# Kernel optimization log

Measured on AMD Instinct MI355X. Metric: run time of the kernel, lower is better.

The kernel has to match this reference:

```python
import jax, jax.numpy as jnp
import numpy as np

B, T, E, H = 2, 2048, 1024, 16
DV = E // H
EPS = 1e-5

def _layernorm(x, g, b):
    m = jnp.mean(x, axis=-1, keepdims=True)
    v = jnp.mean((x - m) ** 2, axis=-1, keepdims=True)
    return (x - m) * jax.lax.rsqrt(v + EPS) * g + b

def setup_inputs() -> dict:
    key = jax.random.key(0)
    ks = jax.random.split(key, 10)
    s = lambda fan_in: 1.0 / np.sqrt(fan_in)
    return {
        "x": jax.random.normal(ks[0], (B, T, E), jnp.float32),
        "wq": jax.random.normal(ks[1], (H, E, DV), jnp.float32) * s(E),
        "wk": jax.random.normal(ks[2], (H, E, DV), jnp.float32) * s(E),
        "wv": jax.random.normal(ks[3], (H, E, DV), jnp.float32) * s(E),
        "w_proj": jax.random.normal(ks[4], (E, E), jnp.float32) * s(E),
        "b_proj": jnp.zeros((E,), jnp.float32),
        "w1": jax.random.normal(ks[5], (E, 4 * E), jnp.float32) * s(E),
        "b1": jnp.zeros((4 * E,), jnp.float32),
        "w2": jax.random.normal(ks[6], (4 * E, E), jnp.float32) * s(4 * E),
        "b2": jnp.zeros((E,), jnp.float32),
        "g1": jnp.ones((E,), jnp.float32),
        "be1": jnp.zeros((E,), jnp.float32),
        "g2": jnp.ones((E,), jnp.float32),
        "be2": jnp.zeros((E,), jnp.float32),
    }

def reference(x, wq, wk, wv, w_proj, b_proj, w1, b1, w2, b2, g1, be1, g2, be2):
    Bc, Tc, C = x.shape
    # --- masked multi-head self-attention on pre-LN input ---
    h = _layernorm(x, g1, be1)
    q = jnp.einsum('bte,hed->bhtd', h, wq)
    k = jnp.einsum('bte,hed->bhtd', h, wk)
    v = jnp.einsum('bte,hed->bhtd', h, wv)
    # NOTE: original scales by C**-0.5 where C = full embed dim (not head dim)
    scores = jnp.einsum('bhtd,bhsd->bhts', q, k) * (C ** -0.5)
    causal = jnp.tril(jnp.ones((Tc, Tc), bool))
    scores = jnp.where(causal, scores, jnp.float32(-jnp.inf))
    probs = jax.nn.softmax(scores, axis=-1)  # dropout is identity in eval
    attn = jnp.einsum('bhts,bhsd->bhtd', probs, v)
    attn = attn.transpose(0, 2, 1, 3).reshape(Bc, Tc, C)
    x = x + (attn @ w_proj + b_proj)
    # --- feed-forward ---
    h2 = _layernorm(x, g2, be2)
    ff = jax.nn.relu(h2 @ w1 + b1) @ w2 + b2
    return x + ff
```

## Files before the change

kernel.cpp:

```cpp
#include <hip/hip_runtime.h>
#include <hip/hip_bf16.h>

typedef __bf16 bf16x8 __attribute__((ext_vector_type(8)));
typedef __bf16 bf16x4 __attribute__((ext_vector_type(4)));
typedef float f32x4 __attribute__((ext_vector_type(4)));

#define T_SEQ 2048
#define EMB 1024
#define NH 16
#define DV 64

__device__ __forceinline__ void gload16(const __bf16* g, __bf16* l) {
    __builtin_amdgcn_global_load_lds(
        (const __attribute__((address_space(1))) unsigned int*)g,
        (__attribute__((address_space(3))) unsigned int*)l, 16, 0, 0);
}

__global__ void transpose_cvt(const float* __restrict__ src, __bf16* __restrict__ dst,
                              int R, int C, long src_bstride, long dst_bstride, float scale) {
    __shared__ float tile[32][33];
    const int b = blockIdx.z;
    const float* s = src + (long)b * src_bstride;
    __bf16* d = dst + (long)b * dst_bstride;
    const int c0 = blockIdx.x * 32, r0 = blockIdx.y * 32;
    #pragma unroll
    for (int i = threadIdx.y; i < 32; i += 8)
        tile[i][threadIdx.x] = s[(long)(r0 + i) * C + c0 + threadIdx.x];
    __syncthreads();
    #pragma unroll
    for (int i = threadIdx.y; i < 32; i += 8)
        d[(long)(c0 + i) * R + r0 + threadIdx.x] = (__bf16)(tile[threadIdx.x][i] * scale);
}

__global__ void vt_transpose(const __bf16* __restrict__ qkv, __bf16* __restrict__ Vt) {
    __shared__ __bf16 tile[64][72];
    const int bh = blockIdx.y, b = bh >> 4, h = bh & 15;
    const int t0 = blockIdx.x * 64;
    const __bf16* src = qkv + (long)b * T_SEQ * 3072 + 2048 + h * 64;
    const int tt = threadIdx.x >> 3, seg = threadIdx.x & 7;
    #pragma unroll
    for (int half = 0; half < 2; half++) {
        const int t = half * 32 + tt;
        bf16x8 v = *reinterpret_cast<const bf16x8*>(src + (long)(t0 + t) * 3072 + seg * 8);
        *reinterpret_cast<bf16x8*>(&tile[t][seg * 8]) = v;
    }
    __syncthreads();
    __bf16* dst = Vt + (long)bh * 64 * T_SEQ + t0;
    #pragma unroll
    for (int half = 0; half < 2; half++) {
        const int d = half * 32 + tt;
        bf16x8 v;
        #pragma unroll
        for (int i = 0; i < 8; i++) v[i] = tile[seg * 8 + i][d];
        *reinterpret_cast<bf16x8*>(dst + (long)d * T_SEQ + seg * 8) = v;
    }
}

__global__ void ln_kernel(const float* __restrict__ x, const float* __restrict__ g,
                          const float* __restrict__ be, __bf16* __restrict__ out) {
    const int row = blockIdx.x;
    const float4 xv = reinterpret_cast<const float4*>(x + (long)row * EMB)[threadIdx.x];
    float s = xv.x + xv.y + xv.z + xv.w;
    float sq = xv.x * xv.x + xv.y * xv.y + xv.z * xv.z + xv.w * xv.w;
    #pragma unroll
    for (int off = 32; off; off >>= 1) { s += __shfl_down(s, off); sq += __shfl_down(sq, off); }
    __shared__ float red[8];
    const int w = threadIdx.x >> 6, lane = threadIdx.x & 63;
    if (lane == 0) { red[w] = s; red[4 + w] = sq; }
    __syncthreads();
    if (threadIdx.x == 0) {
        float st = red[0] + red[1] + red[2] + red[3];
        float sqt = red[4] + red[5] + red[6] + red[7];
        float mean = st * (1.0f / EMB);
        float var = sqt * (1.0f / EMB) - mean * mean;
        red[0] = mean; red[1] = rsqrtf(var + 1e-5f);
    }
    __syncthreads();
    const float mean = red[0], rstd = red[1];
    const float4 gv = reinterpret_cast<const float4*>(g)[threadIdx.x];
    const float4 bv = reinterpret_cast<const float4*>(be)[threadIdx.x];
    bf16x4 o;
    o[0] = (__bf16)((xv.x - mean) * rstd * gv.x + bv.x);
    o[1] = (__bf16)((xv.y - mean) * rstd * gv.y + bv.y);
    o[2] = (__bf16)((xv.z - mean) * rstd * gv.z + bv.z);
    o[3] = (__bf16)((xv.w - mean) * rstd * gv.w + bv.w);
    *reinterpret_cast<bf16x4*>(out + (long)row * EMB + threadIdx.x * 4) = o;
}

template <int RELU, int HAS_BIAS>
__global__ __launch_bounds__(512)
void gemm256(const __bf16* __restrict__ A, const __bf16* __restrict__ BT,
             const float* __restrict__ bias, __bf16* __restrict__ outp,
             int M, int N, int K, int nbx) {
    __shared__ __align__(16) __bf16 lds[3][2][256 * 32];
    const int bid = (int)blockIdx.x;
    const int cpx = (int)gridDim.x >> 3;
    const int wg = (bid & 7) * cpx + (bid >> 3);
    const int bx = wg % nbx, by = wg / nbx;
    const int m0 = by * 256, n0 = bx * 256;
    const int tid = threadIdx.x, wid = tid >> 6, lane = tid & 63;
    const int wr = wid >> 2, wc = wid & 3;
    const int rA = lane & 15, g = lane >> 4, rl = g * 4;
    const int rswz = (g ^ ((rA >> 1) & 3)) * 8;

    const int sr = tid >> 2, ch = tid & 3;
    const int sc = ch ^ ((sr >> 1) & 3);
    const __bf16* Asrc = A + (long)(m0 + sr) * K + sc * 8;
    const __bf16* Bsrc = BT + (long)(n0 + sr) * K + sc * 8;
    const int dOff = sr * 32 + ch * 8;

    auto stage = [&](int t) {
        const int buf = t % 3, k0 = t * 32;
        gload16(Asrc + k0,            &lds[buf][0][dOff]);
        gload16(Asrc + 128 * K + k0,  &lds[buf][0][128 * 32 + dOff]);
        gload16(Bsrc + k0,            &lds[buf][1][dOff]);
        gload16(Bsrc + 128 * K + k0,  &lds[buf][1][128 * 32 + dOff]);
    };

    f32x4 acc[8][4] = {};
    const int NT = K >> 5;
    stage(0); stage(1);
    asm volatile("s_waitcnt vmcnt(4)" ::: "memory");
    __builtin_amdgcn_s_barrier();

    for (int t = 0; t < NT; ++t) {
        const int buf = t % 3;
        if (t + 2 < NT) stage(t + 2);
        const __bf16* Abuf = lds[buf][0];
        const __bf16* Bbuf = lds[buf][1];
        bf16x8 bfr[4], af[8];
        #pragma unroll
        for (int n = 0; n < 4; n++)
            bfr[n] = *reinterpret_cast<const bf16x8*>(Bbuf + (wc * 64 + n * 16 + rA) * 32 + rswz);
        #pragma unroll
        for (int m = 0; m < 4; m++)
            af[m] = *reinterpret_cast<const bf16x8*>(Abuf + (wr * 128 + m * 16 + rA) * 32 + rswz);
        __builtin_amdgcn_s_setprio(1);
        #pragma unroll
        for (int m = 0; m < 4; m++)
            #pragma unroll
            for (int n = 0; n < 4; n++)
                acc[m][n] = __builtin_amdgcn_mfma_f32_16x16x32_bf16(af[m], bfr[n], acc[m][n], 0, 0, 0);
        __builtin_amdgcn_s_setprio(0);
        __builtin_amdgcn_s_barrier();
        #pragma unroll
        for (int m = 4; m < 8; m++)
            af[m] = *reinterpret_cast<const bf16x8*>(Abuf + (wr * 128 + m * 16 + rA) * 32 + rswz);
        __builtin_amdgcn_s_setprio(1);
        #pragma unroll
        for (int m = 4; m < 8; m++)
            #pragma unroll
            for (int n = 0; n < 4; n++)
                acc[m][n] = __builtin_amdgcn_mfma_f32_16x16x32_bf16(af[m], bfr[n], acc[m][n], 0, 0, 0);
        __builtin_amdgcn_s_setprio(0);
        asm volatile("s_waitcnt vmcnt(4)" ::: "memory");
        __builtin_amdgcn_s_barrier();
    }

    #pragma unroll
    for (int m = 0; m < 8; m++) {
        #pragma unroll
        for (int n = 0; n < 4; n++) {
            const int gc = n0 + wc * 64 + n * 16 + rA;
            float bval = 0.0f;
            if (HAS_BIAS) bval = bias[gc];
            #pragma unroll
            for (int r = 0; r < 4; r++) {
                const int gr = m0 + wr * 128 + m * 16 + rl + r;
                float v = acc[m][n][r] + bval;
                if (RELU) v = fmaxf(v, 0.0f);
                outp[(long)gr * N + gc] = (__bf16)v;
            }
        }
    }
}

template <int BN, int OUT_BF16, int RELU, int HAS_BIAS, int HAS_RES>
__global__ __launch_bounds__(256)
void gemm_nt(const __bf16* __restrict__ A, const __bf16* __restrict__ BT,
             const float* __restrict__ bias, const float* __restrict__ res,
             void* __restrict__ outp, int M, int N, int K) {
    constexpr int NFN = BN / 32;
    __shared__ __align__(16) __bf16 As[128 * 64];
    __shared__ __align__(16) __bf16 Bs[BN * 64];
    const int t = threadIdx.x;
    const int w = t >> 6, lane = t & 63;
    const int wm = (w >> 1) * 64, wn = (w & 1) * (BN / 2);
    const int m0 = blockIdx.y * 128, n0 = blockIdx.x * BN;
    const int rA = lane & 15, kA = (lane >> 4) * 8;
    const int swzr = (rA & 7) * 8;
    const int srow = t >> 3;
    const int chunk = t & 7;
    const int schunk = chunk ^ (srow & 7);

    const __bf16* Ab = A + (long)(m0 + srow) * K + schunk * 8;
    const __bf16* Bb = BT + (long)(n0 + srow) * K + schunk * 8;
    __bf16* Asw = As + srow * 64 + chunk * 8;
    __bf16* Bsw = Bs + srow * 64 + chunk * 8;

    f32x4 acc[4][NFN] = {};
    for (int k0 = 0; k0 < K; k0 += 64) {
        #pragma unroll
        for (int i = 0; i < 4; i++)
            gload16(Ab + (long)(32 * i) * K + k0, Asw + 32 * i * 64);
        #pragma unroll
        for (int i = 0; i < BN / 32; i++)
            gload16(Bb + (long)(32 * i) * K + k0, Bsw + 32 * i * 64);
        __syncthreads();
        #pragma unroll
        for (int kk = 0; kk < 2; kk++) {
            bf16x8 af[4], bfr[NFN];
            #pragma unroll
            for (int m = 0; m < 4; m++)
                af[m] = *reinterpret_cast<const bf16x8*>(
                    As + (wm + m * 16 + rA) * 64 + ((kk * 32 + kA) ^ swzr));
            #pragma unroll
            for (int n = 0; n < NFN; n++)
                bfr[n] = *reinterpret_cast<const bf16x8*>(
                    Bs + (wn + n * 16 + rA) * 64 + ((kk * 32 + kA) ^ swzr));
            #pragma unroll
            for (int m = 0; m < 4; m++)
                #pragma unroll
                for (int n = 0; n < NFN; n++)
                    acc[m][n] = __builtin_amdgcn_mfma_f32_16x16x32_bf16(af[m], bfr[n], acc[m][n], 0, 0, 0);
        }
        __syncthreads();
    }
    const int rl = (lane >> 4) * 4, cl = lane & 15;
    #pragma unroll
    for (int m = 0; m < 4; m++) {
        #pragma unroll
        for (int n = 0; n < NFN; n++) {
            const int gc = n0 + wn + n * 16 + cl;
            float bval = 0.0f;
            if (HAS_BIAS) bval = bias[gc];
            #pragma unroll
            for (int r = 0; r < 4; r++) {
                const int gr = m0 + wm + m * 16 + rl + r;
                float v = acc[m][n][r] + bval;
                if (HAS_RES) v += res[(long)gr * N + gc];
                if (RELU) v = fmaxf(v, 0.0f);
                if (OUT_BF16) ((__bf16*)outp)[(long)gr * N + gc] = (__bf16)v;
                else          ((float*)outp)[(long)gr * N + gc] = v;
            }
        }
    }
}

template <int MASKED>
__device__ __forceinline__ void attn_compute(
    const char* __restrict__ Kl, const char* __restrict__ Vl,
    __bf16 (*__restrict__ PsW)[72],
    const bf16x8 (&qf)[2][2], const bf16x8& ones,
    f32x4 (&o)[2][4], f32x4 (&l5)[2], float (&mr)[2][4],
    int kv0, int rA, int g, int rl, int qw)
{
    const int swz = (rA & 7) << 4;
    bf16x8 kf[4][2];
    #pragma unroll
    for (int c = 0; c < 4; c++)
        #pragma unroll
        for (int kc = 0; kc < 2; kc++)
            kf[c][kc] = *reinterpret_cast<const bf16x8*>(
                Kl + (c * 16 + rA) * 128 + ((kc * 64 + g * 16) ^ swz));
    f32x4 sa[2][4];
    __builtin_amdgcn_s_setprio(1);
    #pragma unroll
    for (int rt = 0; rt < 2; rt++)
        #pragma unroll
        for (int c = 0; c < 4; c++) {
            f32x4 acc = {};
            acc = __builtin_amdgcn_mfma_f32_16x16x32_bf16(qf[rt][0], kf[c][0], acc, 0, 0, 0);
            acc = __builtin_amdgcn_mfma_f32_16x16x32_bf16(qf[rt][1], kf[c][1], acc, 0, 0, 0);
            sa[rt][c] = acc;
        }
    __builtin_amdgcn_s_setprio(0);
    #pragma unroll
    for (int rt = 0; rt < 2; rt++) {
        #pragma unroll
        for (int r = 0; r < 4; r++) {
            float s0 = sa[rt][0][r], s1 = sa[rt][1][r], s2 = sa[rt][2][r], s3 = sa[rt][3][r];
            if (MASKED) {
                const int gr = qw + rt * 16 + rl + r;
                if (kv0 + rA > gr)      s0 = -__builtin_inff();
                if (kv0 + 16 + rA > gr) s1 = -__builtin_inff();
                if (kv0 + 32 + rA > gr) s2 = -__builtin_inff();
                if (kv0 + 48 + rA > gr) s3 = -__builtin_inff();
            }
            float tm = fmaxf(fmaxf(s0, s1), fmaxf(s2, s3));
            #pragma unroll
            for (int msk = 1; msk < 16; msk <<= 1) tm = fmaxf(tm, __shfl_xor(tm, msk));
            const float mo = mr[rt][r];
            float mu = mo;
            if (__any(tm > mo + 8.0f)) {
                const float mn = fmaxf(mo, tm);
                mr[rt][r] = mn;
                const float sc = __expf(mo - mn);
                #pragma unroll
                for (int n = 0; n < 4; n++) o[rt][n][r] *= sc;
                l5[rt][r] *= sc;
                mu = mn;
            }
            const float p0 = __expf(s0 - mu);
            const float p1 = __expf(s1 - mu);
            const float p2 = __expf(s2 - mu);
            const float p3 = __expf(s3 - mu);
            const int prow = rt * 16 + rl + r;
            PsW[prow][rA]      = (__bf16)p0;
            PsW[prow][16 + rA] = (__bf16)p1;
            PsW[prow][32 + rA] = (__bf16)p2;
            PsW[prow][48 + rA] = (__bf16)p3;
        }
    }
    asm volatile("s_waitcnt lgkmcnt(0)" ::: "memory");

    bf16x8 ap[2][2];
    #pragma unroll
    for (int rt = 0; rt < 2; rt++)
        #pragma unroll
        for (int ks = 0; ks < 2; ks++)
            ap[rt][ks] = *reinterpret_cast<const bf16x8*>(&PsW[rt * 16 + rA][ks * 32 + g * 8]);
    __builtin_amdgcn_s_setprio(1);
    #pragma unroll
    for (int ks = 0; ks < 2; ks++) {
        #pragma unroll
        for (int rt = 0; rt < 2; rt++)
            l5[rt] = __builtin_amdgcn_mfma_f32_16x16x32_bf16(ap[rt][ks], ones, l5[rt], 0, 0, 0);
        #pragma unroll
        for (int n = 0; n < 4; n++) {
            bf16x8 bv = *reinterpret_cast<const bf16x8*>(
                Vl + (n * 16 + rA) * 128 + ((ks * 64 + g * 16) ^ swz));
            #pragma unroll
            for (int rt = 0; rt < 2; rt++)
                o[rt][n] = __builtin_amdgcn_mfma_f32_16x16x32_bf16(ap[rt][ks], bv, o[rt][n], 0, 0, 0);
        }
    }
    __builtin_amdgcn_s_setprio(0);
}

__global__ __launch_bounds__(256)
void attn_kernel(const __bf16* __restrict__ qkv, const __bf16* __restrict__ Vt,
                 __bf16* __restrict__ attn) {
    __shared__ __bf16 Ks[2][64 * 64];
    __shared__ __bf16 Vs[2][64 * 64];
    __shared__ __bf16 Ps[4][32][72];

    const int bid = (int)blockIdx.x;
    const int xcd = bid & 7, s = bid >> 3;
    const int slot = s >> 5, c = s & 31;
    const int bh = xcd * 4 + slot * 2 + (c >> 4);
    const int t16 = c & 15;
    const int qtile = slot ? t16 : 15 - t16;
    const int b = bh >> 4, h = bh & 15;
    const int q0 = qtile * 128;
    const int w = threadIdx.x >> 6, lane = threadIdx.x & 63;
    const int qw = q0 + w * 32;
    const int rA = lane & 15, g = lane >> 4, rl = g * 4;
    const int srow8 = lane >> 3;
    const int scol = (lane & 7) * 16;
    const int wcol = scol ^ (srow8 << 4);

    const char* qb = (const char*)(qkv + (long)b * T_SEQ * 3072 + h * 64);
    const char* kb = qb + 2048;
    const char* vtb = (const char*)(Vt + (long)bh * 64 * T_SEQ);

    bf16x8 qf[2][2];
    #pragma unroll
    for (int rt = 0; rt < 2; rt++)
        #pragma unroll
        for (int kc = 0; kc < 2; kc++)
            qf[rt][kc] = *reinterpret_cast<const bf16x8*>(
                qb + (long)(qw + rt * 16 + rA) * 6144 + kc * 64 + g * 16);

    bf16x8 ones;
    #pragma unroll
    for (int i = 0; i < 8; i++) ones[i] = (__bf16)1.0f;

    f32x4 o[2][4] = {};
    f32x4 l5[2] = {};
    float mr[2][4];
    #pragma unroll
    for (int rt = 0; rt < 2; rt++)
        #pragma unroll
        for (int r = 0; r < 4; r++) mr[rt][r] = -__builtin_inff();

    const int nsteps = q0 / 64 + 2;
    const int t_avail = qw + 32;
    const int isK = (w < 2);
    const int r0 = (w & 1) * 32 + srow8;

    bf16x8 stg[4];
    auto issue = [&](int kv0) {
        if (isK) {
            #pragma unroll
            for (int i = 0; i < 4; i++)
                stg[i] = *reinterpret_cast<const bf16x8*>(kb + (long)(kv0 + r0 + i * 8) * 6144 + scol);
        } else {
            #pragma unroll
            for (int i = 0; i < 4; i++)
                stg[i] = *reinterpret_cast<const bf16x8*>(vtb + (long)(r0 + i * 8) * 4096 + kv0 * 2 + scol);
        }
    };
    auto lwrite = [&](int buf) {
        char* base = isK ? (char*)Ks[buf] : (char*)Vs[buf];
        #pragma unroll
        for (int i = 0; i < 4; i++)
            *reinterpret_cast<bf16x8*>(base + (r0 + i * 8) * 128 + wcol) = stg[i];
    };

    issue(0);
    lwrite(0);
    __syncthreads();

    for (int t = 0; t < nsteps; ++t) {
        const int kv0 = t * 64, cur = t & 1;
        const bool has_next = (t + 1 < nsteps);
        if (has_next) issue(kv0 + 64);
        if (kv0 < t_avail) {
            if (kv0 + 64 <= qw)
                attn_compute<0>((const char*)Ks[cur], (const char*)Vs[cur], Ps[w],
                                qf, ones, o, l5, mr, kv0, rA, g, rl, qw);
            else
                attn_compute<1>((const char*)Ks[cur], (const char*)Vs[cur], Ps[w],
                                qf, ones, o, l5, mr, kv0, rA, g, rl, qw);
        }
        if (has_next) lwrite(cur ^ 1);
        __syncthreads();
    }

    #pragma unroll
    for (int rt = 0; rt < 2; rt++)
        #pragma unroll
        for (int n = 0; n < 4; n++)
            #pragma unroll
            for (int r = 0; r < 4; r++) {
                const int gr = qw + rt * 16 + rl + r;
                attn[(long)(b * T_SEQ + gr) * EMB + h * 64 + n * 16 + rA] =
                    (__bf16)(o[rt][n][r] / l5[rt][r]);
            }
}

extern "C" void kernel_launch(void* const* d_in, const int* in_sizes, int n_in,
                              void* d_out, int out_size, void* d_ws, size_t ws_size,
                              hipStream_t stream) {
    const float* x      = (const float*)d_in[0];
    const float* wq     = (const float*)d_in[1];
    const float* wk     = (const float*)d_in[2];
    const float* wv     = (const float*)d_in[3];
    const float* w_proj = (const float*)d_in[4];
    const float* b_proj = (const float*)d_in[5];
    const float* w1     = (const float*)d_in[6];
    const float* b1     = (const float*)d_in[7];
    const float* w2     = (const float*)d_in[8];
    const float* b2     = (const float*)d_in[9];
    const float* g1     = (const float*)d_in[10];
    const float* be1    = (const float*)d_in[11];
    const float* g2     = (const float*)d_in[12];
    const float* be2    = (const float*)d_in[13];
    float* out = (float*)d_out;

    char* ws = (char*)d_ws;
    __bf16* WqkvT = (__bf16*)ws;  ws += 3072L * 1024 * 2;
    __bf16* WprojT = (__bf16*)ws; ws += 1024L * 1024 * 2;
    __bf16* W1T = (__bf16*)ws;    ws += 4096L * 1024 * 2;
    __bf16* W2T = (__bf16*)ws;    ws += 1024L * 4096 * 2;
    __bf16* h1  = (__bf16*)ws;    ws += 4096L * 1024 * 2;
    __bf16* qkvb = (__bf16*)ws;
    __bf16* attnb = (__bf16*)(ws + 4096L * 3072 * 2);
    __bf16* ffb = (__bf16*)ws;    ws += 4096L * 3072 * 2 + 4096L * 1024 * 2;
    float* x2 = (float*)ws;
    __bf16* Vt = (__bf16*)ws;

    const dim3 tb(32, 8);
    transpose_cvt<<<dim3(2, 32, 16), tb, 0, stream>>>(wq, WqkvT,                1024, 64, 65536L, 65536L, 0.03125f);
    transpose_cvt<<<dim3(2, 32, 16), tb, 0, stream>>>(wk, WqkvT + 1024L * 1024, 1024, 64, 65536L, 65536L, 1.0f);
    transpose_cvt<<<dim3(2, 32, 16), tb, 0, stream>>>(wv, WqkvT + 2048L * 1024, 1024, 64, 65536L, 65536L, 1.0f);
    transpose_cvt<<<dim3(32, 32, 1),  tb, 0, stream>>>(w_proj, WprojT, 1024, 1024, 0, 0, 1.0f);
    transpose_cvt<<<dim3(128, 32, 1), tb, 0, stream>>>(w1, W1T, 1024, 4096, 0, 0, 1.0f);
    transpose_cvt<<<dim3(32, 128, 1), tb, 0, stream>>>(w2, W2T, 4096, 1024, 0, 0, 1.0f);

    ln_kernel<<<4096, 256, 0, stream>>>(x, g1, be1, h1);
    gemm256<0, 0><<<192, 512, 0, stream>>>(h1, WqkvT, nullptr, qkvb, 4096, 3072, 1024, 12);
    vt_transpose<<<dim3(32, 32), 256, 0, stream>>>(qkvb, Vt);
    attn_kernel<<<512, 256, 0, stream>>>(qkvb, Vt, attnb);
    gemm_nt<64, 0, 0, 1, 1><<<dim3(16, 32), 256, 0, stream>>>(attnb, WprojT, b_proj, x, x2, 4096, 1024, 1024);
    ln_kernel<<<4096, 256, 0, stream>>>(x2, g2, be2, h1);
    gemm256<1, 1><<<256, 512, 0, stream>>>(h1, W1T, b1, ffb, 4096, 4096, 1024, 16);
    gemm_nt<64, 0, 0, 1, 1><<<dim3(16, 32), 256, 0, stream>>>(ffb, W2T, b2, x2, out, 4096, 1024, 4096);
}
```

Measured before the change: 386.6 us.

## Replace gemm_nt with triple-buffered 128x128 pipelined GEMM for proj and FFN2

```diff
diff --git a/kernel.cpp b/kernel.cpp
--- a/kernel.cpp
+++ b/kernel.cpp
@@ -153,7 +153,8 @@
             for (int n = 0; n < 4; n++)
                 acc[m][n] = __builtin_amdgcn_mfma_f32_16x16x32_bf16(af[m], bfr[n], acc[m][n], 0, 0, 0);
         __builtin_amdgcn_s_setprio(0);
-        asm volatile("s_waitcnt vmcnt(4)" ::: "memory");
+        if (t + 3 < NT) asm volatile("s_waitcnt vmcnt(4)" ::: "memory");
+        else            asm volatile("s_waitcnt vmcnt(0)" ::: "memory");
         __builtin_amdgcn_s_barrier();
     }
 
@@ -175,73 +176,75 @@
     }
 }
 
-template <int BN, int OUT_BF16, int RELU, int HAS_BIAS, int HAS_RES>
 __global__ __launch_bounds__(256)
-void gemm_nt(const __bf16* __restrict__ A, const __bf16* __restrict__ BT,
-             const float* __restrict__ bias, const float* __restrict__ res,
-             void* __restrict__ outp, int M, int N, int K) {
-    constexpr int NFN = BN / 32;
-    __shared__ __align__(16) __bf16 As[128 * 64];
-    __shared__ __align__(16) __bf16 Bs[BN * 64];
-    const int t = threadIdx.x;
-    const int w = t >> 6, lane = t & 63;
-    const int wm = (w >> 1) * 64, wn = (w & 1) * (BN / 2);
-    const int m0 = blockIdx.y * 128, n0 = blockIdx.x * BN;
-    const int rA = lane & 15, kA = (lane >> 4) * 8;
-    const int swzr = (rA & 7) * 8;
-    const int srow = t >> 3;
-    const int chunk = t & 7;
-    const int schunk = chunk ^ (srow & 7);
-
-    const __bf16* Ab = A + (long)(m0 + srow) * K + schunk * 8;
-    const __bf16* Bb = BT + (long)(n0 + srow) * K + schunk * 8;
-    __bf16* Asw = As + srow * 64 + chunk * 8;
-    __bf16* Bsw = Bs + srow * 64 + chunk * 8;
-
-    f32x4 acc[4][NFN] = {};
-    for (int k0 = 0; k0 < K; k0 += 64) {
-        #pragma unroll
-        for (int i = 0; i < 4; i++)
-            gload16(Ab + (long)(32 * i) * K + k0, Asw + 32 * i * 64);
-        #pragma unroll
-        for (int i = 0; i < BN / 32; i++)
-            gload16(Bb + (long)(32 * i) * K + k0, Bsw + 32 * i * 64);
-        __syncthreads();
-        #pragma unroll
-        for (int kk = 0; kk < 2; kk++) {
-            bf16x8 af[4], bfr[NFN];
-            #pragma unroll
-            for (int m = 0; m < 4; m++)
-                af[m] = *reinterpret_cast<const bf16x8*>(
-                    As + (wm + m * 16 + rA) * 64 + ((kk * 32 + kA) ^ swzr));
-            #pragma unroll
-            for (int n = 0; n < NFN; n++)
-                bfr[n] = *reinterpret_cast<const bf16x8*>(
-                    Bs + (wn + n * 16 + rA) * 64 + ((kk * 32 + kA) ^ swzr));
-            #pragma unroll
-            for (int m = 0; m < 4; m++)
-                #pragma unroll
-                for (int n = 0; n < NFN; n++)
-                    acc[m][n] = __builtin_amdgcn_mfma_f32_16x16x32_bf16(af[m], bfr[n], acc[m][n], 0, 0, 0);
-        }
-        __syncthreads();
-    }
-    const int rl = (lane >> 4) * 4, cl = lane & 15;
+void gemm128p(const __bf16* __restrict__ A, const __bf16* __restrict__ BT,
+              const float* __restrict__ bias, const float* __restrict__ res,
+              float* __restrict__ outp, int M, int N, int K, int nbx) {
+    __shared__ __align__(16) __bf16 lds[3][2][128 * 32];
+    const int bid = (int)blockIdx.x;
+    const int cpx = (int)gridDim.x >> 3;
+    const int wg = (bid & 7) * cpx + (bid >> 3);
+    const int bx = wg % nbx, by = wg / nbx;
+    const int m0 = by * 128, n0 = bx * 128;
+    const int tid = threadIdx.x, wid = tid >> 6, lane = tid & 63;
+    const int wr = wid >> 1, wc = wid & 1;
+    const int rA = lane & 15, g = lane >> 4, rl = g * 4;
+    const int rswz = (g ^ ((rA >> 1) & 3)) * 8;
+
+    const int sr = tid >> 2, ch = tid & 3;
+    const int sc = ch ^ ((sr >> 1) & 3);
+    const __bf16* Asrc = A + (long)(m0 + sr) * K + sc * 8;
+    const __bf16* Bsrc = BT + (long)(n0 + sr) * K + sc * 8;
+    const int dOff = sr * 32 + ch * 8;
+
+    auto stage = [&](int t) {
+        const int buf = t % 3, k0 = t * 32;
+        gload16(Asrc + k0,           &lds[buf][0][dOff]);
+        gload16(Asrc + 64 * (long)K + k0, &lds[buf][0][64 * 32 + dOff]);
+        gload16(Bsrc + k0,           &lds[buf][1][dOff]);
+        gload16(Bsrc + 64 * (long)K + k0, &lds[buf][1][64 * 32 + dOff]);
+    };
+
+    f32x4 acc[4][4] = {};
+    const int NT = K >> 5;
+    stage(0); stage(1);
+    asm volatile("s_waitcnt vmcnt(4)" ::: "memory");
+    __builtin_amdgcn_s_barrier();
+
+    for (int t = 0; t < NT; ++t) {
+        const int buf = t % 3;
+        if (t + 2 < NT) stage(t + 2);
+        const __bf16* Abuf = lds[buf][0];
+        const __bf16* Bbuf = lds[buf][1];
+        bf16x8 af[4], bfr[4];
+        #pragma unroll
+        for (int n = 0; n < 4; n++)
+            bfr[n] = *reinterpret_cast<const bf16x8*>(Bbuf + (wc * 64 + n * 16 + rA) * 32 + rswz);
+        #pragma unroll
+        for (int m = 0; m < 4; m++)
+            af[m] = *reinterpret_cast<const bf16x8*>(Abuf + (wr * 64 + m * 16 + rA) * 32 + rswz);
+        __builtin_amdgcn_s_setprio(1);
+        #pragma unroll
+        for (int m = 0; m < 4; m++)
+            #pragma unroll
+            for (int n = 0; n < 4; n++)
+                acc[m][n] = __builtin_amdgcn_mfma_f32_16x16x32_bf16(af[m], bfr[n], acc[m][n], 0, 0, 0);
+        __builtin_amdgcn_s_setprio(0);
+        if (t + 3 < NT) asm volatile("s_waitcnt vmcnt(4)" ::: "memory");
+        else            asm volatile("s_waitcnt vmcnt(0)" ::: "memory");
+        __builtin_amdgcn_s_barrier();
+    }
+
     #pragma unroll
     for (int m = 0; m < 4; m++) {
         #pragma unroll
-        for (int n = 0; n < NFN; n++) {
-            const int gc = n0 + wn + n * 16 + cl;
-            float bval = 0.0f;
-            if (HAS_BIAS) bval = bias[gc];
+        for (int n = 0; n < 4; n++) {
+            const int gc = n0 + wc * 64 + n * 16 + rA;
+            const float bval = bias[gc];
             #pragma unroll
             for (int r = 0; r < 4; r++) {
-                const int gr = m0 + wm + m * 16 + rl + r;
-                float v = acc[m][n][r] + bval;
-                if (HAS_RES) v += res[(long)gr * N + gc];
-                if (RELU) v = fmaxf(v, 0.0f);
-                if (OUT_BF16) ((__bf16*)outp)[(long)gr * N + gc] = (__bf16)v;
-                else          ((float*)outp)[(long)gr * N + gc] = v;
+                const int gr = m0 + wr * 64 + m * 16 + rl + r;
+                outp[(long)gr * N + gc] = acc[m][n][r] + bval + res[(long)gr * N + gc];
             }
         }
     }
@@ -483,8 +486,8 @@
     gemm256<0, 0><<<192, 512, 0, stream>>>(h1, WqkvT, nullptr, qkvb, 4096, 3072, 1024, 12);
     vt_transpose<<<dim3(32, 32), 256, 0, stream>>>(qkvb, Vt);
     attn_kernel<<<512, 256, 0, stream>>>(qkvb, Vt, attnb);
-    gemm_nt<64, 0, 0, 1, 1><<<dim3(16, 32), 256, 0, stream>>>(attnb, WprojT, b_proj, x, x2, 4096, 1024, 1024);
+    gemm128p<<<256, 256, 0, stream>>>(attnb, WprojT, b_proj, x, x2, 4096, 1024, 1024, 8);
     ln_kernel<<<4096, 256, 0, stream>>>(x2, g2, be2, h1);
     gemm256<1, 1><<<256, 512, 0, stream>>>(h1, W1T, b1, ffb, 4096, 4096, 1024, 16);
-    gemm_nt<64, 0, 0, 1, 1><<<dim3(16, 32), 256, 0, stream>>>(ffb, W2T, b2, x2, out, 4096, 1024, 4096);
-}
+    gemm128p<<<256, 256, 0, stream>>>(ffb, W2T, b2, x2, out, 4096, 1024, 4096, 8);
+}
```

Measured after the change: 377.3 us. -2.4%, faster.
